# Kernel tuning notes

Measured on AMD Instinct MI355X. Metric: run time of the kernel, lower is better.

The kernel has to match this reference:

```python
import jax, jax.numpy as jnp
import numpy as np

N, IN_C, OUT_C, H, CF = 4096, 256, 256, 8, 6
D = OUT_C // H

def setup_inputs() -> dict:
    key = jax.random.key(0)
    ks = jax.random.split(key, 8)
    x = jax.random.normal(ks[0], (N, IN_C), dtype=jnp.float32)
    positions = jax.random.normal(ks[1], (N, 3), dtype=jnp.float32)
    curv_feats = jax.random.normal(ks[2], (N, CF), dtype=jnp.float32)
    adj = jax.random.randint(ks[3], (N, N), 0, 2, dtype=jnp.int32)
    W = jax.random.normal(ks[4], (OUT_C, IN_C), dtype=jnp.float32) * 0.05
    a_l = jax.random.normal(ks[5], (H, D), dtype=jnp.float32) * 0.1
    a_r = jax.random.normal(ks[6], (H, D), dtype=jnp.float32) * 0.1
    Wc = jax.random.normal(ks[7], (H, CF), dtype=jnp.float32) * 0.1
    gate = jnp.asarray(0.1, dtype=jnp.float32)
    return {"x": x, "positions": positions, "curv_feats": curv_feats,
            "adj": adj, "W": W, "a_l": a_l, "a_r": a_r, "Wc": Wc, "gate": gate}

def reference(x, positions, curv_feats, adj, W, a_l, a_r, Wc, gate):
    n = x.shape[0]
    h = (x @ W.T).reshape(n, H, D)                       # (N,H,D)
    e_l = jnp.einsum('nhd,hd->nh', h, a_l)               # (N,H)
    e_r = jnp.einsum('nhd,hd->nh', h, a_r)               # (N,H)
    logits = jax.nn.leaky_relu(e_l[:, None, :] + e_r[None, :, :], negative_slope=0.2)  # (N,N,H)
    curv_pair = jnp.abs(curv_feats[:, None, :] - curv_feats[None, :, :])  # (N,N,CF)
    curv_bias = jnp.einsum('ijf,hf->ijh', curv_pair, Wc)                  # (N,N,H)
    logits = logits + gate * curv_bias
    mask = (adj > 0)[:, :, None]                          # (N,N,1)
    logits = jnp.where(mask, logits, jnp.float32(-1e9))
    attn = jax.nn.softmax(logits, axis=1)                 # softmax over j (dim=1)
    out = jnp.einsum('ijh,jhd->ihd', attn, h)             # (N,H,D)
    return out.reshape(n, H * D)
```

## Files before the change

kernel.cpp:

```cpp
#include <hip/hip_runtime.h>

#define NN 4096
#define HC 8
#define DC 32
#define OC 256
#define KC 256
#define CF 6

typedef _Float16 f16_t;
typedef f16_t f16x2 __attribute__((ext_vector_type(2)));
typedef f16_t f16x8 __attribute__((ext_vector_type(8)));
typedef __fp16 hh2 __attribute__((ext_vector_type(2)));
typedef float f32x4 __attribute__((ext_vector_type(4)));
typedef float f32x2 __attribute__((ext_vector_type(2)));
typedef unsigned u32x4 __attribute__((ext_vector_type(4)));

#if defined(__has_builtin)
#if __has_builtin(__builtin_amdgcn_exp2f)
#define EXP2F(x) __builtin_amdgcn_exp2f(x)
#else
#define EXP2F(x) exp2f(x)
#endif
#else
#define EXP2F(x) exp2f(x)
#endif

union HU { f16x2 h; unsigned u; };

__global__ __launch_bounds__(256) void prep_all(const float* __restrict__ x,
                                                const float* __restrict__ W,
                                                const float* __restrict__ a_l,
                                                const float* __restrict__ a_r,
                                                const int* __restrict__ adj,
                                                const float* __restrict__ cfeat,
                                                const float* __restrict__ Wc,
                                                const float* __restrict__ gate,
                                                float* __restrict__ e_l2,
                                                f16_t* __restrict__ erP,
                                                f16_t* __restrict__ hT2,
                                                unsigned* __restrict__ adjb,
                                                float* __restrict__ cfT,
                                                f16_t* __restrict__ cfP,
                                                float* __restrict__ Wc2) {
  __shared__ float As[16][68];
  __shared__ float Bs[16][36];
  __shared__ float Ct[DC][65];
  const float LOG2E = 1.44269504088896340736f;
  const int t = threadIdx.x;
  const int bid = blockIdx.x;

  if (bid >= 512) {
    const int pb = bid - 512;
    const int ptid = pb * 256 + t;
    const int lane = t & 63;
    const int wv = pb * 4 + (t >> 6);
    int v[32];
#pragma unroll
    for (int u = 0; u < 32; ++u) {
      int g = wv * 32 + u;
      v[u] = adj[(size_t)(g >> 6) * NN + (g & 63) * 64 + lane];
    }
#pragma unroll
    for (int u = 0; u < 32; ++u) {
      int g = wv * 32 + u;
      unsigned long long m = __ballot(v[u] > 0);
      if (lane == 0) *(unsigned long long*)(adjb + (g >> 6) * 128 + (g & 63) * 2) = m;
    }
    if (ptid < NN * CF) {
      int j = ptid / CF, f = ptid - j * CF;
      float vv = cfeat[ptid];
      cfT[f * NN + j] = vv;
      int cc = j >> 5, qq = (j >> 3) & 3, tt = j & 7;
      cfP[((cc * 4 + qq) * CF + f) * 8 + tt] = (f16_t)vv;
    }
    if (ptid < HC * CF) Wc2[ptid] = Wc[ptid] * gate[0] * LOG2E;
    return;
  }

  const int i0 = (bid & 63) * 64;
  const int head = bid >> 6;
  const int c0 = head * DC;
  const int tx = t & 7;
  const int ty = t >> 3;
  const int lr = t >> 2;
  const int lk = (t & 3) * 4;

  float acc[2][4] = {};
  f32x4 av = *(const f32x4*)&x[(size_t)(i0 + lr) * KC + lk];
  f32x4 wv = {};
  if (t < 128) wv = *(const f32x4*)&W[(size_t)(c0 + (t >> 2)) * KC + lk];
  for (int kk = 0; kk < KC; kk += 16) {
    __syncthreads();
    As[lk + 0][lr] = av[0]; As[lk + 1][lr] = av[1];
    As[lk + 2][lr] = av[2]; As[lk + 3][lr] = av[3];
    if (t < 128) {
      int br = t >> 2;
      Bs[lk + 0][br] = wv[0]; Bs[lk + 1][br] = wv[1];
      Bs[lk + 2][br] = wv[2]; Bs[lk + 3][br] = wv[3];
    }
    __syncthreads();
    if (kk + 16 < KC) {
      av = *(const f32x4*)&x[(size_t)(i0 + lr) * KC + kk + 16 + lk];
      if (t < 128) wv = *(const f32x4*)&W[(size_t)(c0 + (t >> 2)) * KC + kk + 16 + lk];
    }
#pragma unroll
    for (int k = 0; k < 16; ++k) {
      f32x2 a = *(const f32x2*)&As[k][ty * 2];
      f32x4 b = *(const f32x4*)&Bs[k][tx * 4];
#pragma unroll
      for (int r = 0; r < 2; ++r)
#pragma unroll
        for (int u = 0; u < 4; ++u)
          acc[r][u] += a[r] * b[u];
    }
  }

  f32x4 al4 = *(const f32x4*)&a_l[c0 + tx * 4];
  f32x4 ar4 = *(const f32x4*)&a_r[c0 + tx * 4];
#pragma unroll
  for (int r = 0; r < 2; ++r) {
    float el = acc[r][0] * al4[0] + acc[r][1] * al4[1] +
               acc[r][2] * al4[2] + acc[r][3] * al4[3];
    float er = acc[r][0] * ar4[0] + acc[r][1] * ar4[1] +
               acc[r][2] * ar4[2] + acc[r][3] * ar4[3];
    el += __shfl_xor(el, 1, 64); el += __shfl_xor(el, 2, 64); el += __shfl_xor(el, 4, 64);
    er += __shfl_xor(er, 1, 64); er += __shfl_xor(er, 2, 64); er += __shfl_xor(er, 4, 64);
    if (tx == 0) {
      int j = i0 + ty * 2 + r;
      e_l2[j * HC + head] = el * LOG2E;
      int cc = j >> 5, qq = (j >> 3) & 3, tt = j & 7;
      erP[((cc * 4 + qq) * HC + head) * 8 + tt] = (f16_t)(er * LOG2E);
    }
  }

#pragma unroll
  for (int r = 0; r < 2; ++r)
#pragma unroll
    for (int u = 0; u < 4; ++u)
      Ct[tx * 4 + u][ty * 2 + r] = acc[r][u];
  __syncthreads();
  const size_t base = (size_t)head * (NN / 32) * 1024 + (size_t)(bid & 63) * 2048;
#pragma unroll
  for (int rep = 0; rep < 8; ++rep) {
    int idx = rep * 256 + t;
    int dd = (idx >> 3) & 31;
    int jl = (idx >> 10) * 32 + ((idx >> 8) & 3) * 8 + (idx & 7);
    hT2[base + idx] = (f16_t)Ct[dd][jl];
  }
}

__global__ __launch_bounds__(256, 4) void attn(const unsigned* __restrict__ adjb,
                                               const float* __restrict__ e_l2,
                                               const float* __restrict__ cfT,
                                               const float* __restrict__ Wc2,
                                               const u32x4* __restrict__ cfP4,
                                               const u32x4* __restrict__ erP4,
                                               const f16_t* __restrict__ hT2,
                                               float* __restrict__ out) {
  __shared__ float Obuf[16][64];
  __shared__ float Sbuf[16][2];
  const int tid = threadIdx.x;
  const int w = tid >> 6;
  const int lane = tid & 63;
  const int il = lane & 15;
  const int quad = lane >> 4;
  const int ibase = blockIdx.x * 16;
  const int hg = blockIdx.y;
  const int i = ibase + il;

  for (int idx = tid; idx < 16 * 64; idx += 256) (&Obuf[0][0])[idx] = 0.f;
  if (tid < 32) (&Sbuf[0][0])[tid] = 0.f;
  __syncthreads();

  f16x2 cfi2h[CF];
#pragma unroll
  for (int f = 0; f < CF; ++f) {
    f16_t v = (f16_t)cfT[f * NN + i];
    cfi2h[f] = (f16x2){v, v};
  }
  f16x2 elh[2];
  {
    f32x2 e0 = *(const f32x2*)&e_l2[i * HC + hg * 2];
#pragma unroll
    for (int u = 0; u < 2; ++u) { f16_t v = (f16_t)e0[u]; elh[u] = (f16x2){v, v}; }
  }
  f16x2 wch[2][CF];
#pragma unroll
  for (int h = 0; h < 2; ++h)
#pragma unroll
    for (int f = 0; f < CF; ++f) {
      f16_t v = (f16_t)Wc2[(hg * 2 + h) * CF + f];
      wch[h][f] = (f16x2){v, v};
    }
  const f16x2 lslope = (f16x2){(f16_t)0.2f, (f16_t)0.2f};

  f32x4 acc[2][2];
#pragma unroll
  for (int h = 0; h < 2; ++h)
#pragma unroll
    for (int d = 0; d < 2; ++d) acc[h][d] = (f32x4){0.f, 0.f, 0.f, 0.f};
  float S[2] = {0.f, 0.f};

  const f16_t* hTbase = hT2 + (size_t)hg * 2 * ((NN / 32) * 1024) + quad * 256 + il * 8;
  const u32x4* cfb = cfP4 + quad * CF;
  const u32x4* erb = erP4 + quad * HC + hg * 2;
  const unsigned* adjrow = adjb + i * 128;

  u32x4 cfc[CF];
#pragma unroll
  for (int f = 0; f < CF; ++f) cfc[f] = cfb[w * (4 * CF) + f];
  u32x4 erc[2];
#pragma unroll
  for (int h = 0; h < 2; ++h) erc[h] = erb[w * (4 * HC) + h];
  unsigned mc = adjrow[w];

#pragma unroll 2
  for (int c = w; c < NN / 32; c += 4) {
    const f16_t* bp0 = hTbase + c * 1024;
    const f16_t* bp1 = bp0 + (NN / 32) * 1024;
    f16x8 b00 = *(const f16x8*)bp0;
    f16x8 b01 = *(const f16x8*)(bp0 + 128);
    f16x8 b10 = *(const f16x8*)bp1;
    f16x8 b11 = *(const f16x8*)(bp1 + 128);

    f16x2 arg[2][4];
#pragma unroll
    for (int p = 0; p < 4; ++p) {
      f16x2 bias0 = (f16x2){(f16_t)0.f, (f16_t)0.f};
      f16x2 bias1 = (f16x2){(f16_t)0.f, (f16_t)0.f};
#pragma unroll
      for (int f = 0; f < CF; ++f) {
        HU cu; cu.u = cfc[f][p];
        f16x2 d = cfi2h[f] - cu.h;
        f16x2 ad = __builtin_elementwise_max(d, -d);
        bias0 = __builtin_elementwise_fma(ad, wch[0][f], bias0);
        bias1 = __builtin_elementwise_fma(ad, wch[1][f], bias1);
      }
#pragma unroll
      for (int h = 0; h < 2; ++h) {
        HU eu; eu.u = erc[h][p];
        f16x2 s = elh[h] + eu.h;
        f16x2 lk = __builtin_elementwise_max(s, lslope * s);
        arg[h][p] = lk + (h ? bias1 : bias0);
      }
    }
    const unsigned m8 = (mc >> (quad * 8)) & 0xffu;

    {
      const int cn = (c + 4) & (NN / 32 - 1);
#pragma unroll
      for (int f = 0; f < CF; ++f) cfc[f] = cfb[cn * (4 * CF) + f];
#pragma unroll
      for (int h = 0; h < 2; ++h) erc[h] = erb[cn * (4 * HC) + h];
      mc = adjrow[cn];
    }

    union { f16x8 v; unsigned u[4]; } af[2];
#pragma unroll
    for (int p = 0; p < 4; ++p) {
      const unsigned b0 = (m8 >> (2 * p)) & 1u;
      const unsigned b1 = (m8 >> (2 * p + 1)) & 1u;
#pragma unroll
      for (int h = 0; h < 2; ++h) {
        float lo = (float)arg[h][p][0];
        float hi = (float)arg[h][p][1];
        float e0 = b0 ? EXP2F(lo) : 0.f;
        float e1 = b1 ? EXP2F(hi) : 0.f;
        S[h] += e0 + e1;
        union { hh2 r; unsigned u; } cv;
        cv.r = __builtin_amdgcn_cvt_pkrtz(e0, e1);
        af[h].u[p] = cv.u;
      }
    }

#pragma unroll
    for (int h = 0; h < 2; ++h) {
      acc[h][0] = __builtin_amdgcn_mfma_f32_16x16x32_f16(af[h].v, h ? b10 : b00, acc[h][0], 0, 0, 0);
      acc[h][1] = __builtin_amdgcn_mfma_f32_16x16x32_f16(af[h].v, h ? b11 : b01, acc[h][1], 0, 0, 0);
    }
  }

#pragma unroll
  for (int h = 0; h < 2; ++h) {
    float v = S[h];
    v += __shfl_xor(v, 16, 64);
    v += __shfl_xor(v, 32, 64);
    if (quad == 0) atomicAdd(&Sbuf[il][h], v);
  }
#pragma unroll
  for (int h = 0; h < 2; ++h)
#pragma unroll
    for (int dh = 0; dh < 2; ++dh)
#pragma unroll
      for (int r = 0; r < 4; ++r)
        atomicAdd(&Obuf[quad * 4 + r][h * DC + dh * 16 + il], acc[h][dh][r]);
  __syncthreads();

  for (int idx = tid; idx < 16 * 64; idx += 256) {
    int row = idx >> 6;
    int colg = idx & 63;
    out[(size_t)(ibase + row) * OC + hg * 64 + colg] =
        Obuf[row][colg] / Sbuf[row][colg >> 5];
  }
}

extern "C" void kernel_launch(void* const* d_in, const int* in_sizes, int n_in,
                              void* d_out, int out_size, void* d_ws, size_t ws_size,
                              hipStream_t stream) {
  const float* x    = (const float*)d_in[0];
  const float* cfeat= (const float*)d_in[2];
  const int*   adj  = (const int*)d_in[3];
  const float* W    = (const float*)d_in[4];
  const float* a_l  = (const float*)d_in[5];
  const float* a_r  = (const float*)d_in[6];
  const float* Wc   = (const float*)d_in[7];
  const float* gate = (const float*)d_in[8];
  float* out = (float*)d_out;

  char* ws = (char*)d_ws;
  f16_t*    hT2  = (f16_t*)ws;
  unsigned* adjb = (unsigned*)(ws + (2u << 20));
  float*    e_l2 = (float*)(ws + (4u << 20));
  float*    cfT  = (float*)(ws + (4u << 20) + (128u << 10));
  float*    Wc2  = (float*)(ws + (4u << 20) + (256u << 10));
  f16_t*    cfP  = (f16_t*)(ws + (4u << 20) + (320u << 10));
  f16_t*    erP  = (f16_t*)(ws + (4u << 20) + (384u << 10));

  prep_all<<<2560, 256, 0, stream>>>(x, W, a_l, a_r, adj, cfeat, Wc, gate,
                                     e_l2, erP, hT2, adjb, cfT, cfP, Wc2);
  attn<<<dim3(NN / 16, 4), 256, 0, stream>>>(adjb, e_l2, cfT, Wc2,
                                             (const u32x4*)cfP, (const u32x4*)erP,
                                             hT2, out);
}
```

Before: 187.5 us.

## Fold adjacency mask into fp16 bias, use half exp2, sum denominator via MFMA

The attention loop now encodes masked entries as -inf in the fp16 bias and computes exp2 directly in half precision, dropping the fp32 conversions, the per-element branches and the packed convert. The softmax denominator is accumulated by an extra MFMA against a ones vector rather than scalar adds followed by shuffles. The prep kernel is split into separate GEMM and packing launches. Risks: fp16 exp2 precision and overflow, an added MFMA per head per iteration, and one more kernel launch.

Result: slower. 195.8 us (+4.4%).

```diff
diff --git a/kernel.cpp b/kernel.cpp
--- a/kernel.cpp
+++ b/kernel.cpp
@@ -10,73 +10,27 @@
 typedef _Float16 f16_t;
 typedef f16_t f16x2 __attribute__((ext_vector_type(2)));
 typedef f16_t f16x8 __attribute__((ext_vector_type(8)));
-typedef __fp16 hh2 __attribute__((ext_vector_type(2)));
 typedef float f32x4 __attribute__((ext_vector_type(4)));
 typedef float f32x2 __attribute__((ext_vector_type(2)));
 typedef unsigned u32x4 __attribute__((ext_vector_type(4)));
 
-#if defined(__has_builtin)
-#if __has_builtin(__builtin_amdgcn_exp2f)
-#define EXP2F(x) __builtin_amdgcn_exp2f(x)
-#else
-#define EXP2F(x) exp2f(x)
-#endif
-#else
-#define EXP2F(x) exp2f(x)
-#endif
-
 union HU { f16x2 h; unsigned u; };
 
-__global__ __launch_bounds__(256) void prep_all(const float* __restrict__ x,
-                                                const float* __restrict__ W,
-                                                const float* __restrict__ a_l,
-                                                const float* __restrict__ a_r,
-                                                const int* __restrict__ adj,
-                                                const float* __restrict__ cfeat,
-                                                const float* __restrict__ Wc,
-                                                const float* __restrict__ gate,
-                                                float* __restrict__ e_l2,
-                                                f16_t* __restrict__ erP,
-                                                f16_t* __restrict__ hT2,
-                                                unsigned* __restrict__ adjb,
-                                                float* __restrict__ cfT,
-                                                f16_t* __restrict__ cfP,
-                                                float* __restrict__ Wc2) {
+extern "C" __device__ _Float16 __ocml_exp2_f16(_Float16);
+
+__global__ __launch_bounds__(256) void prep_gemm(const float* __restrict__ x,
+                                                 const float* __restrict__ W,
+                                                 const float* __restrict__ a_l,
+                                                 const float* __restrict__ a_r,
+                                                 float* __restrict__ e_l2,
+                                                 f16_t* __restrict__ erP,
+                                                 f16_t* __restrict__ hT2) {
   __shared__ float As[16][68];
   __shared__ float Bs[16][36];
   __shared__ float Ct[DC][65];
   const float LOG2E = 1.44269504088896340736f;
   const int t = threadIdx.x;
   const int bid = blockIdx.x;
-
-  if (bid >= 512) {
-    const int pb = bid - 512;
-    const int ptid = pb * 256 + t;
-    const int lane = t & 63;
-    const int wv = pb * 4 + (t >> 6);
-    int v[32];
-#pragma unroll
-    for (int u = 0; u < 32; ++u) {
-      int g = wv * 32 + u;
-      v[u] = adj[(size_t)(g >> 6) * NN + (g & 63) * 64 + lane];
-    }
-#pragma unroll
-    for (int u = 0; u < 32; ++u) {
-      int g = wv * 32 + u;
-      unsigned long long m = __ballot(v[u] > 0);
-      if (lane == 0) *(unsigned long long*)(adjb + (g >> 6) * 128 + (g & 63) * 2) = m;
-    }
-    if (ptid < NN * CF) {
-      int j = ptid / CF, f = ptid - j * CF;
-      float vv = cfeat[ptid];
-      cfT[f * NN + j] = vv;
-      int cc = j >> 5, qq = (j >> 3) & 3, tt = j & 7;
-      cfP[((cc * 4 + qq) * CF + f) * 8 + tt] = (f16_t)vv;
-    }
-    if (ptid < HC * CF) Wc2[ptid] = Wc[ptid] * gate[0] * LOG2E;
-    return;
-  }
-
   const int i0 = (bid & 63) * 64;
   const int head = bid >> 6;
   const int c0 = head * DC;
@@ -147,6 +101,42 @@
     int jl = (idx >> 10) * 32 + ((idx >> 8) & 3) * 8 + (idx & 7);
     hT2[base + idx] = (f16_t)Ct[dd][jl];
   }
+}
+
+__global__ __launch_bounds__(256) void prep_pack(const int* __restrict__ adj,
+                                                 const float* __restrict__ cfeat,
+                                                 const float* __restrict__ Wc,
+                                                 const float* __restrict__ gate,
+                                                 unsigned* __restrict__ adjb,
+                                                 float* __restrict__ cfT,
+                                                 f16_t* __restrict__ cfP,
+                                                 float* __restrict__ Wc2) {
+  const float LOG2E = 1.44269504088896340736f;
+  const int t = threadIdx.x;
+  const int pb = blockIdx.x;
+  const int ptid = pb * 256 + t;
+  const int lane = t & 63;
+  const int wv = pb * 4 + (t >> 6);
+  int v[32];
+#pragma unroll
+  for (int u = 0; u < 32; ++u) {
+    int g = wv * 32 + u;
+    v[u] = adj[(size_t)(g >> 6) * NN + (g & 63) * 64 + lane];
+  }
+#pragma unroll
+  for (int u = 0; u < 32; ++u) {
+    int g = wv * 32 + u;
+    unsigned long long m = __ballot(v[u] > 0);
+    if (lane == 0) *(unsigned long long*)(adjb + (g >> 6) * 128 + (g & 63) * 2) = m;
+  }
+  if (ptid < NN * CF) {
+    int j = ptid / CF, f = ptid - j * CF;
+    float vv = cfeat[ptid];
+    cfT[f * NN + j] = vv;
+    int cc = j >> 5, qq = (j >> 3) & 3, tt = j & 7;
+    cfP[((cc * 4 + qq) * CF + f) * 8 + tt] = (f16_t)vv;
+  }
+  if (ptid < HC * CF) Wc2[ptid] = Wc[ptid] * gate[0] * LOG2E;
 }
 
 __global__ __launch_bounds__(256, 4) void attn(const unsigned* __restrict__ adjb,
@@ -193,13 +183,17 @@
       wch[h][f] = (f16x2){v, v};
     }
   const f16x2 lslope = (f16x2){(f16_t)0.2f, (f16_t)0.2f};
+  const f16x8 onesB = {(f16_t)1.f, (f16_t)1.f, (f16_t)1.f, (f16_t)1.f,
+                       (f16_t)1.f, (f16_t)1.f, (f16_t)1.f, (f16_t)1.f};
 
   f32x4 acc[2][2];
 #pragma unroll
   for (int h = 0; h < 2; ++h)
 #pragma unroll
     for (int d = 0; d < 2; ++d) acc[h][d] = (f32x4){0.f, 0.f, 0.f, 0.f};
-  float S[2] = {0.f, 0.f};
+  f32x4 Sacc[2];
+#pragma unroll
+  for (int h = 0; h < 2; ++h) Sacc[h] = (f32x4){0.f, 0.f, 0.f, 0.f};
 
   const f16_t* hTbase = hT2 + (size_t)hg * 2 * ((NN / 32) * 1024) + quad * 256 + il * 8;
   const u32x4* cfb = cfP4 + quad * CF;
@@ -223,11 +217,16 @@
     f16x8 b10 = *(const f16x8*)bp1;
     f16x8 b11 = *(const f16x8*)(bp1 + 128);
 
+    const unsigned m8 = (mc >> (quad * 8)) & 0xffu;
+
     f16x2 arg[2][4];
 #pragma unroll
     for (int p = 0; p < 4; ++p) {
-      f16x2 bias0 = (f16x2){(f16_t)0.f, (f16_t)0.f};
-      f16x2 bias1 = (f16x2){(f16_t)0.f, (f16_t)0.f};
+      HU mb;
+      mb.u = (((m8 >> (2 * p)) & 1u) ? 0u : 0xFC00u) |
+             (((m8 >> (2 * p + 1)) & 1u) ? 0u : 0xFC000000u);
+      f16x2 bias0 = mb.h;
+      f16x2 bias1 = mb.h;
 #pragma unroll
       for (int f = 0; f < CF; ++f) {
         HU cu; cu.u = cfc[f][p];
@@ -244,7 +243,6 @@
         arg[h][p] = lk + (h ? bias1 : bias0);
       }
     }
-    const unsigned m8 = (mc >> (quad * 8)) & 0xffu;
 
     {
       const int cn = (c + 4) & (NN / 32 - 1);
@@ -258,18 +256,14 @@
     union { f16x8 v; unsigned u[4]; } af[2];
 #pragma unroll
     for (int p = 0; p < 4; ++p) {
-      const unsigned b0 = (m8 >> (2 * p)) & 1u;
-      const unsigned b1 = (m8 >> (2 * p + 1)) & 1u;
 #pragma unroll
       for (int h = 0; h < 2; ++h) {
-        float lo = (float)arg[h][p][0];
-        float hi = (float)arg[h][p][1];
-        float e0 = b0 ? EXP2F(lo) : 0.f;
-        float e1 = b1 ? EXP2F(hi) : 0.f;
-        S[h] += e0 + e1;
-        union { hh2 r; unsigned u; } cv;
-        cv.r = __builtin_amdgcn_cvt_pkrtz(e0, e1);
-        af[h].u[p] = cv.u;
+        f16x2 a = arg[h][p];
+        f16x2 r;
+        r[0] = __ocml_exp2_f16(a[0]);
+        r[1] = __ocml_exp2_f16(a[1]);
+        HU pu; pu.h = r;
+        af[h].u[p] = pu.u;
       }
     }
 
@@ -277,15 +271,16 @@
     for (int h = 0; h < 2; ++h) {
       acc[h][0] = __builtin_amdgcn_mfma_f32_16x16x32_f16(af[h].v, h ? b10 : b00, acc[h][0], 0, 0, 0);
       acc[h][1] = __builtin_amdgcn_mfma_f32_16x16x32_f16(af[h].v, h ? b11 : b01, acc[h][1], 0, 0, 0);
-    }
-  }
-
-#pragma unroll
-  for (int h = 0; h < 2; ++h) {
-    float v = S[h];
-    v += __shfl_xor(v, 16, 64);
-    v += __shfl_xor(v, 32, 64);
-    if (quad == 0) atomicAdd(&Sbuf[il][h], v);
+      Sacc[h] = __builtin_amdgcn_mfma_f32_16x16x32_f16(af[h].v, onesB, Sacc[h], 0, 0, 0);
+    }
+  }
+
+  if (il == 0) {
+#pragma unroll
+    for (int h = 0; h < 2; ++h)
+#pragma unroll
+      for (int r = 0; r < 4; ++r)
+        atomicAdd(&Sbuf[quad * 4 + r][h], Sacc[h][r]);
   }
 #pragma unroll
   for (int h = 0; h < 2; ++h)
@@ -326,8 +321,8 @@
   f16_t*    cfP  = (f16_t*)(ws + (4u << 20) + (320u << 10));
   f16_t*    erP  = (f16_t*)(ws + (4u << 20) + (384u << 10));
 
-  prep_all<<<2560, 256, 0, stream>>>(x, W, a_l, a_r, adj, cfeat, Wc, gate,
-                                     e_l2, erP, hT2, adjb, cfT, cfP, Wc2);
+  prep_gemm<<<512, 256, 0, stream>>>(x, W, a_l, a_r, e_l2, erP, hT2);
+  prep_pack<<<2048, 256, 0, stream>>>(adj, cfeat, Wc, gate, adjb, cfT, cfP, Wc2);
   attn<<<dim3(NN / 16, 4), 256, 0, stream>>>(adjb, e_l2, cfT, Wc2,
                                              (const u32x4*)cfP, (const u32x4*)erP,
                                              hT2, out);
```
